# Optimization experiments

Hardware: AMD Instinct MI355X
Metric: run time of the kernel (lower is better)

## Reference

```python
import jax, jax.numpy as jnp
import numpy as np

K = 3
STRIDE = 1
PAD = 1

def conv2d(x, w, b, stride, padding):
    out = jax.lax.conv_general_dilated(x, w, (stride, stride), [(padding, padding), (padding, padding)],
                                       dimension_numbers=('NCHW', 'OIHW', 'NCHW'))
    if b is not None:
        out = out + b[None, :, None, None]
    return out

def deform_conv2d(x, offset, mask, weight, stride, padding):
    # torchvision-style modulated deformable conv (offset_groups=1, groups=1)
    B, C, H, W = x.shape
    C2 = weight.shape[0]
    KK = K * K
    Hout, Wout = offset.shape[2], offset.shape[3]
    off = offset.reshape(B, KK, 2, Hout, Wout)  # (dy, dx) pairs per kernel tap
    ky = jnp.repeat(jnp.arange(K), K)  # kernel row per tap [KK]
    kx = jnp.tile(jnp.arange(K), K)    # kernel col per tap [KK]
    base_y = (jnp.arange(Hout) * stride - padding).astype(jnp.float32)
    base_x = (jnp.arange(Wout) * stride - padding).astype(jnp.float32)
    py = off[:, :, 0] + ky[None, :, None, None] + base_y[None, None, :, None]  # [B,KK,Hout,Wout]
    px = off[:, :, 1] + kx[None, :, None, None] + base_x[None, None, None, :]
    y0f = jnp.floor(py); x0f = jnp.floor(px)
    ly = py - y0f; lx = px - x0f
    y0 = y0f.astype(jnp.int32); x0 = x0f.astype(jnp.int32)
    xf = x.reshape(B, C, H * W)

    def corner(yi, xi, wgt):
        valid = (yi >= 0) & (yi < H) & (xi >= 0) & (xi < W)
        idx = (jnp.clip(yi, 0, H - 1) * W + jnp.clip(xi, 0, W - 1)).reshape(B, -1)  # [B, KK*Hout*Wout]
        v = jax.vmap(lambda xb, ib: xb[:, ib])(xf, idx)  # [B, C, KK*Hout*Wout]
        return v * (wgt * valid).reshape(B, 1, -1)

    val = (corner(y0, x0, (1.0 - ly) * (1.0 - lx))
           + corner(y0, x0 + 1, (1.0 - ly) * lx)
           + corner(y0 + 1, x0, ly * (1.0 - lx))
           + corner(y0 + 1, x0 + 1, ly * lx))
    val = val * mask.reshape(B, 1, -1)  # modulation per (tap, spatial)
    val = val.reshape(B, C, KK, Hout, Wout)
    out = jnp.einsum('bckhw,ock->bohw', val, weight.reshape(C2, C, KK))
    return out

def setup_inputs() -> dict:
    key = jax.random.key(0)
    ks = jax.random.split(key, 6)
    B, C1, C2, H, W = 8, 256, 256, 64, 64
    x = jax.random.normal(ks[0], (B, C1, H, W), jnp.float32)
    offset_w = jax.random.normal(ks[1], (2 * K * K, C1, K, K), jnp.float32) * 0.01
    offset_b = jax.random.normal(ks[2], (2 * K * K,), jnp.float32) * 0.5
    mod_w = jax.random.normal(ks[3], (K * K, C1, K, K), jnp.float32) * 0.01
    mod_b = jnp.zeros((K * K,), jnp.float32)
    reg_w = jax.random.normal(ks[4], (C2, C1, K, K), jnp.float32) * np.float32(1.0 / np.sqrt(C1 * K * K))
    return {"x": x, "offset_w": offset_w, "offset_b": offset_b, "mod_w": mod_w, "mod_b": mod_b, "reg_w": reg_w}

def reference(x, offset_w, offset_b, mod_w, mod_b, reg_w):
    h, w = x.shape[2], x.shape[3]
    max_offset = max(h, w) / 4.0
    offset = jnp.clip(conv2d(x, offset_w, offset_b, STRIDE, PAD), -max_offset, max_offset)
    modulator = jax.nn.sigmoid(conv2d(x, mod_w, mod_b, STRIDE, PAD))
    return deform_conv2d(x, offset, modulator, reg_w, STRIDE, PAD)
```

## Files before the change

kernel.cpp:

```cpp
#include <hip/hip_runtime.h>
#include <math.h>

#define BB 8
#define CIN 256
#define COUT 256
#define HH 64
#define WW 64
#define OCM 27
#define KTOT 2304
#define NKT 72

typedef unsigned int u32;
typedef unsigned short u16;
typedef _Float16 f16;

#define WS_XBF 0
#define WS_W2 16777216
#define WS_W2OM 17956864
#define WS_OFFMOD 18104320

__device__ __forceinline__ u16 f2h(float f) {
    f16 h = (f16)f;
    return __builtin_bit_cast(u16, h);
}

typedef __attribute__((address_space(1))) const unsigned int* gptr_t;
typedef __attribute__((address_space(3))) unsigned int* lptr_t;
__device__ __forceinline__ void gl2lds16(const void* g, void* l) {
    __builtin_amdgcn_global_load_lds((gptr_t)g, (lptr_t)l, 16, 0, 0);
}

typedef __attribute__((ext_vector_type(8))) f16 frag;
typedef __attribute__((ext_vector_type(2))) f16 h2;
typedef __attribute__((ext_vector_type(4))) float f4;

__device__ __forceinline__ int sw_off(int row, int oct) {
    return (row << 5) + ((oct ^ ((row >> 1) & 3)) << 3);
}

#define BARRIER_RAW() do { asm volatile("" ::: "memory"); \
    __builtin_amdgcn_s_barrier(); asm volatile("" ::: "memory"); } while (0)

__global__ __launch_bounds__(256) void k_nhwc3(const float* __restrict__ x,
                                               u16* __restrict__ xbf) {
    const int y = blockIdx.x, b = blockIdx.y;
    __shared__ float T[64][65];
    const int t = threadIdx.x;
    const int wl = t & 63, g = t >> 6;
    const int pr = wl & 31, wsub = wl >> 5;
    u32* xo = (u32*)xbf;
    for (int c0 = 0; c0 < 256; c0 += 64) {
#pragma unroll
        for (int i = 0; i < 16; ++i) {
            int c = g + i * 4;
            T[c][wl] = x[(((size_t)(b * 256 + c0 + c)) << 12) + (y << 6) + wl];
        }
        __syncthreads();
#pragma unroll
        for (int j = 0; j < 8; ++j) {
            int w = j * 8 + g * 2 + wsub;
            u32 v = (u32)f2h(T[2 * pr][w]) | ((u32)f2h(T[2 * pr + 1][w]) << 16);
            xo[((((size_t)b << 12) + (y << 6) + w) << 7) + (c0 >> 1) + pr] = v;
        }
        __syncthreads();
    }
}

__global__ void k_pack_w2(const float* __restrict__ rw, u16* __restrict__ w2) {
    int o = blockIdx.x * blockDim.x + threadIdx.x;
    if (o >= NKT * COUT * 32) return;
    int kk = o & 31;
    int n = (o >> 5) & 255;
    int kt = o >> 13;
    int k = kt * 32 + kk;
    int tap = k >> 8;
    int c = k & 255;
    w2[o] = f2h(rw[n * KTOT + c * 9 + tap]);
}

__global__ void k_pack_w2om(const float* __restrict__ ow, const float* __restrict__ mw,
                            u16* __restrict__ w2om) {
    int o = blockIdx.x * blockDim.x + threadIdx.x;
    if (o >= NKT * 32 * 32) return;
    int kk = o & 31;
    int oc = (o >> 5) & 31;
    int kt = o >> 10;
    int k = kt * 32 + kk;
    int tap = k >> 8;
    int c = k & 255;
    float v = 0.f;
    if (oc < 18) v = ow[oc * KTOT + c * 9 + tap];
    else if (oc < 27) v = mw[(oc - 18) * KTOT + c * 9 + tap];
    w2om[o] = f2h(v);
}

__global__ __launch_bounds__(512, 4) void k_offmod6(
    const u16* __restrict__ xbf, const u16* __restrict__ w2om,
    const float* __restrict__ ob, const float* __restrict__ mb,
    float* __restrict__ offmod)
{
    const int b = blockIdx.x & 7, h = blockIdx.x >> 3;
    const int t = threadIdx.x;
    const int lane = t & 63, wv = t >> 6;
    const int hf = wv >> 2;
    const int wl4 = wv & 3;
    const int th = t & 255;
    const int fr = lane & 15, q = lane >> 4;
    const int wm = wl4 << 4;
    const int mg = th >> 2, oct = th & 3;

    __shared__ u16 AsB[2][2][64 * 32];
    __shared__ u16 BsB[2][2][32 * 32];
    __shared__ float red[64][33];

    const u16* xb = xbf + ((size_t)b << 20);
    const int kbase = hf * 36;

    auto loadA = [&](int kt, uint4* r) {
        int tap = kt >> 3;
        int yy = h + tap / 3 - 1, xx = mg + tap % 3 - 1;
        int c0 = ((kt & 7) << 5) + (oct << 3);
        uint4 v = make_uint4(0, 0, 0, 0);
        if ((unsigned)yy < HH && (unsigned)xx < WW)
            v = *(const uint4*)(xb + (((size_t)yy << 6) + xx) * 256 + c0);
        *r = v;
    };
    auto loadB = [&](int kt, uint4* r) {
        if (th < 128) *r = *(const uint4*)(w2om + (size_t)kt * 1024 + (th >> 2) * 32 + (th & 3) * 8);
    };
    auto storeAB = [&](int buf, uint4* rA, uint4* rB) {
        *(uint4*)&AsB[hf][buf][sw_off(mg, oct)] = *rA;
        if (th < 128) *(uint4*)&BsB[hf][buf][sw_off(th >> 2, th & 3)] = *rB;
    };

    f4 acc[2];
    acc[0] = (f4){0.f, 0.f, 0.f, 0.f};
    acc[1] = (f4){0.f, 0.f, 0.f, 0.f};

    uint4 rA0, rB0, rA1, rB1;
    loadA(kbase, &rA0); loadB(kbase, &rB0);
    storeAB(0, &rA0, &rB0);
    loadA(kbase + 1, &rA1); loadB(kbase + 1, &rB1);
    asm volatile("s_waitcnt lgkmcnt(0)" ::: "memory");

    auto body = [&](int i, int p, uint4* cA, uint4* cB, uint4* nA, uint4* nB) {
        BARRIER_RAW();
        frag a  = *(const frag*)&AsB[hf][p][sw_off(wm + fr, q)];
        frag b0 = *(const frag*)&BsB[hf][p][sw_off(fr, q)];
        frag b1 = *(const frag*)&BsB[hf][p][sw_off(16 + fr, q)];
        if (i + 2 < 36) { loadA(kbase + i + 2, nA); loadB(kbase + i + 2, nB); }
        if (i + 1 < 36) storeAB(1 - p, cA, cB);
        acc[0] = __builtin_amdgcn_mfma_f32_16x16x32_f16(a, b0, acc[0], 0, 0, 0);
        acc[1] = __builtin_amdgcn_mfma_f32_16x16x32_f16(a, b1, acc[1], 0, 0, 0);
        asm volatile("s_waitcnt lgkmcnt(0)" ::: "memory");
    };
    for (int i = 0; i < 36; i += 2) {
        body(i, 0, &rA1, &rB1, &rA0, &rB0);
        body(i + 1, 1, &rA0, &rB0, &rA1, &rB1);
    }

    if (hf == 1) {
#pragma unroll
        for (int ni = 0; ni < 2; ++ni)
#pragma unroll
            for (int r = 0; r < 4; ++r)
                red[wm + q * 4 + r][ni * 16 + fr] = acc[ni][r];
    }
    __syncthreads();
    if (hf == 0) {
#pragma unroll
        for (int ni = 0; ni < 2; ++ni) {
            int oc = ni * 16 + fr;
            if (oc >= OCM) continue;
            bool is_off = oc < 18;
            float bias = is_off ? ob[oc] : mb[oc - 18];
            float4 v;
            float* vp = (float*)&v;
#pragma unroll
            for (int r = 0; r < 4; ++r) {
                float s = acc[ni][r] + red[wm + q * 4 + r][oc] + bias;
                vp[r] = is_off ? fminf(fmaxf(s, -16.f), 16.f)
                               : 1.f / (1.f + __expf(-s));
            }
            *(float4*)&offmod[(((size_t)b * OCM + oc) << 12) + (h << 6) + wm + q * 4] = v;
        }
    }
}

__global__ __launch_bounds__(1024, 4) void k_deform8(
    const u16* __restrict__ xbf, const float* __restrict__ offmod,
    const u16* __restrict__ w2, float* __restrict__ out)
{
    const int t = threadIdx.x;
    const int b = blockIdx.x & 7, hp = blockIdx.x >> 3;
    const int h0 = hp << 1;
    const int lane = t & 63, wv = t >> 6;

    __shared__ uint4 STAB[9][128];
    __shared__ u16 AsB[2][128 * 32];
    __shared__ u16 BsB[2][256 * 32];

    const float* om = offmod + (size_t)b * OCM * 4096;
    for (int e = t; e < 9 * 128; e += 1024) {
        int m = e & 127, tap = e >> 7;
        int hh = h0 + (m >> 6), ww = m & 63;
        float dy = om[(tap * 2) * 4096 + hh * 64 + ww];
        float dx = om[(tap * 2 + 1) * 4096 + hh * 64 + ww];
        float mv = om[(18 + tap) * 4096 + hh * 64 + ww];
        float py = dy + (float)(tap / 3) + (float)(hh - 1);
        float px = dx + (float)(tap % 3) + (float)(ww - 1);
        float y0f = floorf(py), x0f = floorf(px);
        float ly = py - y0f, lx = px - x0f;
        int y0 = (int)y0f, x0 = (int)x0f;
        int   ysr[2] = {y0, y0 + 1};
        int   xsr[2] = {x0, x0 + 1};
        float wy[2] = {1.f - ly, ly};
        float wx[2] = {1.f - lx, lx};
        u16 idx[4]; f16 wgt[4];
#pragma unroll
        for (int r = 0; r < 4; ++r) {
            int yy = ysr[r >> 1], xx = xsr[r & 1];
            bool ok = ((unsigned)yy < HH) && ((unsigned)xx < WW);
            int yc = min(max(yy, 0), HH - 1);
            int xc = min(max(xx, 0), WW - 1);
            idx[r] = (u16)(yc * WW + xc);
            wgt[r] = (f16)(ok ? (wy[r >> 1] * wx[r & 1] * mv) : 0.f);
        }
        uint4 tv;
        tv.x = (u32)idx[0] | ((u32)idx[1] << 16);
        tv.y = (u32)idx[2] | ((u32)idx[3] << 16);
        h2 w01 = {wgt[0], wgt[1]};
        h2 w23 = {wgt[2], wgt[3]};
        tv.z = __builtin_bit_cast(u32, w01);
        tv.w = __builtin_bit_cast(u32, w23);
        STAB[tap][m] = tv;
    }
    __syncthreads();

    if (wv < 8) {
        const int fr = lane & 15, q = lane >> 4;
        const int wn = wv << 5;

        f4 acc[8][2];
#pragma unroll
        for (int mi = 0; mi < 8; ++mi) {
            acc[mi][0] = (f4){0.f, 0.f, 0.f, 0.f};
            acc[mi][1] = (f4){0.f, 0.f, 0.f, 0.f};
        }

        for (int kt = 0; kt < NKT; ++kt) {
            const int p = kt & 1;
            BARRIER_RAW();
            frag b0 = *(const frag*)&BsB[p][sw_off(wn + fr, q)];
            frag b1 = *(const frag*)&BsB[p][sw_off(wn + 16 + fr, q)];
#pragma unroll
            for (int mi = 0; mi < 8; ++mi) {
                frag a = *(const frag*)&AsB[p][sw_off(mi * 16 + fr, q)];
                acc[mi][0] = __builtin_amdgcn_mfma_f32_16x16x32_f16(a, b0, acc[mi][0], 0, 0, 0);
                acc[mi][1] = __builtin_amdgcn_mfma_f32_16x16x32_f16(a, b1, acc[mi][1], 0, 0, 0);
            }
        }

#pragma unroll
        for (int ni = 0; ni < 2; ++ni) {
            int n_g = wn + ni * 16 + fr;
            float* outn = out + (((size_t)b * COUT + n_g) << 12) + (h0 << 6);
#pragma unroll
            for (int mi = 0; mi < 8; ++mi) {
                int off = ((mi >> 2) << 6) + ((mi & 3) << 4) + (q << 2);
                *(float4*)&outn[off] = make_float4(acc[mi][ni][0], acc[mi][ni][1],
                                                   acc[mi][ni][2], acc[mi][ni][3]);
            }
        }
    } else {
        const int pt = t - 512;
        const int mg = pt >> 2, oct = pt & 3;
        const int pwv = wv - 8;
        const int ko_sw = (lane & 3) ^ ((lane >> 3) & 3);
        const u16* xpl = xbf + ((size_t)b << 20);

        auto stageB = [&](int kt, int buf) {
            const u16* src = w2 + ((size_t)kt << 13);
#pragma unroll
            for (int j = 0; j < 2; ++j) {
                int base = (pwv << 5) + (j << 4);
                int n = base + (lane >> 2);
                u16* dst = &BsB[buf][base << 5];
                gl2lds16(src + n * 32 + ko_sw * 8, dst);
            }
        };
        auto loadCorners = [&](int kt, uint4 (&cr)[4]) {
            int tap = kt >> 3;
            int c0 = ((kt & 7) << 5) + (oct << 3);
            uint2 iv = *(const uint2*)&STAB[tap][mg];
            const u16* base = xpl + c0;
            cr[0] = *(const uint4*)(base + ((size_t)(iv.x & 0xFFFFu) << 8));
            cr[1] = *(const uint4*)(base + ((size_t)(iv.x >> 16) << 8));
            cr[2] = *(const uint4*)(base + ((size_t)(iv.y & 0xFFFFu) << 8));
            cr[3] = *(const uint4*)(base + ((size_t)(iv.y >> 16) << 8));
        };
        auto interpStore = [&](int kt, int buf, uint4 (&cr)[4]) {
            int tap = kt >> 3;
            uint2 wvp = *(const uint2*)(((const u32*)&STAB[tap][mg]) + 2);
            h2 w01 = __builtin_bit_cast(h2, wvp.x);
            h2 w23 = __builtin_bit_cast(h2, wvp.y);
            h2 s0 = {w01[0], w01[0]};
            h2 s1 = {w01[1], w01[1]};
            h2 s2 = {w23[0], w23[0]};
            h2 s3 = {w23[1], w23[1]};
            const u32* c0p = (const u32*)&cr[0];
            const u32* c1p = (const u32*)&cr[1];
            const u32* c2p = (const u32*)&cr[2];
            const u32* c3p = (const u32*)&cr[3];
            u32 o[4];
#pragma unroll
            for (int jj = 0; jj < 4; ++jj) {
                h2 v = s0 * __builtin_bit_cast(h2, c0p[jj]);
                v += s1 * __builtin_bit_cast(h2, c1p[jj]);
                v += s2 * __builtin_bit_cast(h2, c2p[jj]);
                v += s3 * __builtin_bit_cast(h2, c3p[jj]);
                o[jj] = __builtin_bit_cast(u32, v);
            }
            *(uint4*)&AsB[buf][sw_off(mg, oct)] = make_uint4(o[0], o[1], o[2], o[3]);
        };

        uint4 cr0[4], cr1[4], cr2[4];
        stageB(0, 0);
        loadCorners(0, cr0);
        loadCorners(1, cr1);
        loadCorners(2, cr2);
        interpStore(0, 0, cr0);
        asm volatile("s_waitcnt lgkmcnt(0)" ::: "memory");

        auto pstep = [&](int kt, int p, uint4 (&cur)[4], uint4 (&nxt)[4]) {
            if (kt + 2 < NKT) asm volatile("s_waitcnt vmcnt(4)" ::: "memory");
            else              asm volatile("s_waitcnt vmcnt(0)" ::: "memory");
            BARRIER_RAW();
            if (kt + 1 < NKT) stageB(kt + 1, 1 - p);
            if (kt + 3 < NKT) loadCorners(kt + 3, nxt);
            if (kt + 1 < NKT) interpStore(kt + 1, 1 - p, cur);
            asm volatile("s_waitcnt lgkmcnt(0)" ::: "memory");
        };
        for (int kt = 0; kt < NKT; kt += 6) {
            pstep(kt,     0, cr1, cr0);
            pstep(kt + 1, 1, cr2, cr1);
            pstep(kt + 2, 0, cr0, cr2);
            pstep(kt + 3, 1, cr1, cr0);
            pstep(kt + 4, 0, cr2, cr1);
            pstep(kt + 5, 1, cr0, cr2);
        }
    }
}

extern "C" void kernel_launch(void* const* d_in, const int* in_sizes, int n_in,
                              void* d_out, int out_size, void* d_ws, size_t ws_size,
                              hipStream_t stream) {
    const float* x  = (const float*)d_in[0];
    const float* ow = (const float*)d_in[1];
    const float* ob = (const float*)d_in[2];
    const float* mw = (const float*)d_in[3];
    const float* mb = (const float*)d_in[4];
    const float* rw = (const float*)d_in[5];
    float* out = (float*)d_out;
    char* ws = (char*)d_ws;

    u16*   xbf    = (u16*)(ws + WS_XBF);
    u16*   w2     = (u16*)(ws + WS_W2);
    u16*   w2om   = (u16*)(ws + WS_W2OM);
    float* offmod = (float*)(ws + WS_OFFMOD);

    k_nhwc3<<<dim3(HH, BB), 256, 0, stream>>>(x, xbf);
    k_pack_w2<<<(NKT * COUT * 32 + 255) / 256, 256, 0, stream>>>(rw, w2);
    k_pack_w2om<<<(NKT * 32 * 32 + 255) / 256, 256, 0, stream>>>(ow, mw, w2om);
    k_offmod6<<<dim3(512), 512, 0, stream>>>(xbf, w2om, ob, mb, offmod);
    k_deform8<<<dim3(256), 1024, 0, stream>>>(xbf, offmod, w2, out);
}
```

Baseline: 169.8 us.

## Fuse prep kernels into one launch and retile deform MFMA warps 4x4

```diff
diff --git a/kernel.cpp b/kernel.cpp
--- a/kernel.cpp
+++ b/kernel.cpp
@@ -41,57 +41,56 @@
 #define BARRIER_RAW() do { asm volatile("" ::: "memory"); \
     __builtin_amdgcn_s_barrier(); asm volatile("" ::: "memory"); } while (0)
 
-__global__ __launch_bounds__(256) void k_nhwc3(const float* __restrict__ x,
-                                               u16* __restrict__ xbf) {
-    const int y = blockIdx.x, b = blockIdx.y;
-    __shared__ float T[64][65];
+__global__ __launch_bounds__(256) void k_prep(
+    const float* __restrict__ x, const float* __restrict__ rw,
+    const float* __restrict__ ow, const float* __restrict__ mw,
+    u16* __restrict__ xbf, u16* __restrict__ w2, u16* __restrict__ w2om)
+{
+    const int bid = blockIdx.x;
     const int t = threadIdx.x;
-    const int wl = t & 63, g = t >> 6;
-    const int pr = wl & 31, wsub = wl >> 5;
-    u32* xo = (u32*)xbf;
-    for (int c0 = 0; c0 < 256; c0 += 64) {
-#pragma unroll
-        for (int i = 0; i < 16; ++i) {
-            int c = g + i * 4;
-            T[c][wl] = x[(((size_t)(b * 256 + c0 + c)) << 12) + (y << 6) + wl];
-        }
-        __syncthreads();
-#pragma unroll
-        for (int j = 0; j < 8; ++j) {
-            int w = j * 8 + g * 2 + wsub;
-            u32 v = (u32)f2h(T[2 * pr][w]) | ((u32)f2h(T[2 * pr + 1][w]) << 16);
-            xo[((((size_t)b << 12) + (y << 6) + w) << 7) + (c0 >> 1) + pr] = v;
-        }
-        __syncthreads();
-    }
-}
-
-__global__ void k_pack_w2(const float* __restrict__ rw, u16* __restrict__ w2) {
-    int o = blockIdx.x * blockDim.x + threadIdx.x;
-    if (o >= NKT * COUT * 32) return;
-    int kk = o & 31;
-    int n = (o >> 5) & 255;
-    int kt = o >> 13;
-    int k = kt * 32 + kk;
-    int tap = k >> 8;
-    int c = k & 255;
-    w2[o] = f2h(rw[n * KTOT + c * 9 + tap]);
-}
-
-__global__ void k_pack_w2om(const float* __restrict__ ow, const float* __restrict__ mw,
-                            u16* __restrict__ w2om) {
-    int o = blockIdx.x * blockDim.x + threadIdx.x;
-    if (o >= NKT * 32 * 32) return;
-    int kk = o & 31;
-    int oc = (o >> 5) & 31;
-    int kt = o >> 10;
-    int k = kt * 32 + kk;
-    int tap = k >> 8;
-    int c = k & 255;
-    float v = 0.f;
-    if (oc < 18) v = ow[oc * KTOT + c * 9 + tap];
-    else if (oc < 27) v = mw[(oc - 18) * KTOT + c * 9 + tap];
-    w2om[o] = f2h(v);
+    if (bid < 512) {
+        const int y = bid & 63, b = bid >> 6;
+        __shared__ float T[64][65];
+        const int wl = t & 63, g = t >> 6;
+        const int pr = wl & 31, wsub = wl >> 5;
+        u32* xo = (u32*)xbf;
+        for (int c0 = 0; c0 < 256; c0 += 64) {
+#pragma unroll
+            for (int i = 0; i < 16; ++i) {
+                int c = g + i * 4;
+                T[c][wl] = x[(((size_t)(b * 256 + c0 + c)) << 12) + (y << 6) + wl];
+            }
+            __syncthreads();
+#pragma unroll
+            for (int j = 0; j < 8; ++j) {
+                int w = j * 8 + g * 2 + wsub;
+                u32 v = (u32)f2h(T[2 * pr][w]) | ((u32)f2h(T[2 * pr + 1][w]) << 16);
+                xo[((((size_t)b << 12) + (y << 6) + w) << 7) + (c0 >> 1) + pr] = v;
+            }
+            __syncthreads();
+        }
+    } else if (bid < 2816) {
+        int o = ((bid - 512) << 8) + t;
+        int kk = o & 31;
+        int n = (o >> 5) & 255;
+        int kt = o >> 13;
+        int k = kt * 32 + kk;
+        int tap = k >> 8;
+        int c = k & 255;
+        w2[o] = f2h(rw[n * KTOT + c * 9 + tap]);
+    } else {
+        int o = ((bid - 2816) << 8) + t;
+        int kk = o & 31;
+        int oc = (o >> 5) & 31;
+        int kt = o >> 10;
+        int k = kt * 32 + kk;
+        int tap = k >> 8;
+        int c = k & 255;
+        float v = 0.f;
+        if (oc < 18) v = ow[oc * KTOT + c * 9 + tap];
+        else if (oc < 27) v = mw[(oc - 18) * KTOT + c * 9 + tap];
+        w2om[o] = f2h(v);
+    }
 }
 
 __global__ __launch_bounds__(512, 4) void k_offmod6(
@@ -187,7 +186,7 @@
     }
 }
 
-__global__ __launch_bounds__(1024, 4) void k_deform8(
+__global__ __launch_bounds__(1024, 4) void k_deform9(
     const u16* __restrict__ xbf, const float* __restrict__ offmod,
     const u16* __restrict__ w2, float* __restrict__ out)
 {
@@ -239,37 +238,44 @@
 
     if (wv < 8) {
         const int fr = lane & 15, q = lane >> 4;
-        const int wn = wv << 5;
-
-        f4 acc[8][2];
-#pragma unroll
-        for (int mi = 0; mi < 8; ++mi) {
-            acc[mi][0] = (f4){0.f, 0.f, 0.f, 0.f};
-            acc[mi][1] = (f4){0.f, 0.f, 0.f, 0.f};
-        }
+        const int wn4 = wv & 3;
+        const int wm2 = wv >> 2;
+
+        f4 acc[4][4];
+#pragma unroll
+        for (int mi = 0; mi < 4; ++mi)
+#pragma unroll
+            for (int ni = 0; ni < 4; ++ni) acc[mi][ni] = (f4){0.f, 0.f, 0.f, 0.f};
 
         for (int kt = 0; kt < NKT; ++kt) {
             const int p = kt & 1;
             BARRIER_RAW();
-            frag b0 = *(const frag*)&BsB[p][sw_off(wn + fr, q)];
-            frag b1 = *(const frag*)&BsB[p][sw_off(wn + 16 + fr, q)];
-#pragma unroll
-            for (int mi = 0; mi < 8; ++mi) {
-                frag a = *(const frag*)&AsB[p][sw_off(mi * 16 + fr, q)];
-                acc[mi][0] = __builtin_amdgcn_mfma_f32_16x16x32_f16(a, b0, acc[mi][0], 0, 0, 0);
-                acc[mi][1] = __builtin_amdgcn_mfma_f32_16x16x32_f16(a, b1, acc[mi][1], 0, 0, 0);
-            }
-        }
-
-#pragma unroll
-        for (int ni = 0; ni < 2; ++ni) {
-            int n_g = wn + ni * 16 + fr;
-            float* outn = out + (((size_t)b * COUT + n_g) << 12) + (h0 << 6);
-#pragma unroll
-            for (int mi = 0; mi < 8; ++mi) {
-                int off = ((mi >> 2) << 6) + ((mi & 3) << 4) + (q << 2);
-                *(float4*)&outn[off] = make_float4(acc[mi][ni][0], acc[mi][ni][1],
-                                                   acc[mi][ni][2], acc[mi][ni][3]);
+            frag av[4], bv[4];
+#pragma unroll
+            for (int mi = 0; mi < 4; ++mi)
+                av[mi] = *(const frag*)&AsB[p][sw_off((wm2 << 6) + mi * 16 + fr, q)];
+#pragma unroll
+            for (int ni = 0; ni < 4; ++ni)
+                bv[ni] = *(const frag*)&BsB[p][sw_off((wn4 << 6) + ni * 16 + fr, q)];
+            __builtin_amdgcn_s_setprio(1);
+#pragma unroll
+            for (int mi = 0; mi < 4; ++mi)
+#pragma unroll
+                for (int ni = 0; ni < 4; ++ni)
+                    acc[mi][ni] = __builtin_amdgcn_mfma_f32_16x16x32_f16(
+                        av[mi], bv[ni], acc[mi][ni], 0, 0, 0);
+            __builtin_amdgcn_s_setprio(0);
+        }
+
+#pragma unroll
+        for (int ni = 0; ni < 4; ++ni) {
+            int n_g = (wn4 << 6) + ni * 16 + fr;
+            float* outn = out + (((size_t)b * COUT + n_g) << 12) + ((h0 + wm2) << 6);
+#pragma unroll
+            for (int mi = 0; mi < 4; ++mi) {
+                *(float4*)&outn[mi * 16 + (q << 2)] =
+                    make_float4(acc[mi][ni][0], acc[mi][ni][1],
+                                acc[mi][ni][2], acc[mi][ni][3]);
             }
         }
     } else {
@@ -369,9 +375,7 @@
     u16*   w2om   = (u16*)(ws + WS_W2OM);
     float* offmod = (float*)(ws + WS_OFFMOD);
 
-    k_nhwc3<<<dim3(HH, BB), 256, 0, stream>>>(x, xbf);
-    k_pack_w2<<<(NKT * COUT * 32 + 255) / 256, 256, 0, stream>>>(rw, w2);
-    k_pack_w2om<<<(NKT * 32 * 32 + 255) / 256, 256, 0, stream>>>(ow, mw, w2om);
+    k_prep<<<dim3(3104), 256, 0, stream>>>(x, rw, ow, mw, xbf, w2, w2om);
     k_offmod6<<<dim3(512), 512, 0, stream>>>(xbf, w2om, ob, mb, offmod);
-    k_deform8<<<dim3(256), 1024, 0, stream>>>(xbf, offmod, w2, out);
-}
+    k_deform9<<<dim3(256), 1024, 0, stream>>>(xbf, offmod, w2, out);
+}
```

Result: faster. 165.0 us (-2.8%).

## Fuse offset/mask conv into deform kernel and merge prep kernels

Applied to the files above, without the earlier changes.

```diff
diff --git a/kernel.cpp b/kernel.cpp
--- a/kernel.cpp
+++ b/kernel.cpp
@@ -17,7 +17,6 @@
 #define WS_XBF 0
 #define WS_W2 16777216
 #define WS_W2OM 17956864
-#define WS_OFFMOD 18104320
 
 __device__ __forceinline__ u16 f2h(float f) {
     f16 h = (f16)f;
@@ -41,15 +40,21 @@
 #define BARRIER_RAW() do { asm volatile("" ::: "memory"); \
     __builtin_amdgcn_s_barrier(); asm volatile("" ::: "memory"); } while (0)
 
-__global__ __launch_bounds__(256) void k_nhwc3(const float* __restrict__ x,
-                                               u16* __restrict__ xbf) {
-    const int y = blockIdx.x, b = blockIdx.y;
-    __shared__ float T[64][65];
+__global__ __launch_bounds__(256) void k_prep(
+    const float* __restrict__ x, const float* __restrict__ rw,
+    const float* __restrict__ ow, const float* __restrict__ mw,
+    u16* __restrict__ xbf, u16* __restrict__ w2, u16* __restrict__ w2om)
+{
+    const int bid = blockIdx.x;
     const int t = threadIdx.x;
-    const int wl = t & 63, g = t >> 6;
-    const int pr = wl & 31, wsub = wl >> 5;
-    u32* xo = (u32*)xbf;
-    for (int c0 = 0; c0 < 256; c0 += 64) {
+    if (bid < 2048) {
+        const int c0 = (bid & 3) << 6;
+        const int y = (bid >> 2) & 63;
+        const int b = bid >> 8;
+        __shared__ float T[64][65];
+        const int wl = t & 63, g = t >> 6;
+        const int pr = wl & 31, wsub = wl >> 5;
+        u32* xo = (u32*)xbf;
 #pragma unroll
         for (int i = 0; i < 16; ++i) {
             int c = g + i * 4;
@@ -62,151 +67,138 @@
             u32 v = (u32)f2h(T[2 * pr][w]) | ((u32)f2h(T[2 * pr + 1][w]) << 16);
             xo[((((size_t)b << 12) + (y << 6) + w) << 7) + (c0 >> 1) + pr] = v;
         }
-        __syncthreads();
+    } else if (bid < 4352) {
+        int o = ((bid - 2048) << 8) + t;
+        int kk = o & 31;
+        int n = (o >> 5) & 255;
+        int kt = o >> 13;
+        int k = kt * 32 + kk;
+        int tap = k >> 8;
+        int c = k & 255;
+        w2[o] = f2h(rw[n * KTOT + c * 9 + tap]);
+    } else {
+        int o = ((bid - 4352) << 8) + t;
+        int kk = o & 31;
+        int oc = (o >> 5) & 31;
+        int kt = o >> 10;
+        int k = kt * 32 + kk;
+        int tap = k >> 8;
+        int c = k & 255;
+        float v = 0.f;
+        if (oc < 18) v = ow[oc * KTOT + c * 9 + tap];
+        else if (oc < 27) v = mw[(oc - 18) * KTOT + c * 9 + tap];
+        w2om[o] = f2h(v);
     }
 }
 
-__global__ void k_pack_w2(const float* __restrict__ rw, u16* __restrict__ w2) {
-    int o = blockIdx.x * blockDim.x + threadIdx.x;
-    if (o >= NKT * COUT * 32) return;
-    int kk = o & 31;
-    int n = (o >> 5) & 255;
-    int kt = o >> 13;
-    int k = kt * 32 + kk;
-    int tap = k >> 8;
-    int c = k & 255;
-    w2[o] = f2h(rw[n * KTOT + c * 9 + tap]);
-}
-
-__global__ void k_pack_w2om(const float* __restrict__ ow, const float* __restrict__ mw,
-                            u16* __restrict__ w2om) {
-    int o = blockIdx.x * blockDim.x + threadIdx.x;
-    if (o >= NKT * 32 * 32) return;
-    int kk = o & 31;
-    int oc = (o >> 5) & 31;
-    int kt = o >> 10;
-    int k = kt * 32 + kk;
-    int tap = k >> 8;
-    int c = k & 255;
-    float v = 0.f;
-    if (oc < 18) v = ow[oc * KTOT + c * 9 + tap];
-    else if (oc < 27) v = mw[(oc - 18) * KTOT + c * 9 + tap];
-    w2om[o] = f2h(v);
-}
-
-__global__ __launch_bounds__(512, 4) void k_offmod6(
+__global__ __launch_bounds__(1024, 4) void k_fused(
     const u16* __restrict__ xbf, const u16* __restrict__ w2om,
     const float* __restrict__ ob, const float* __restrict__ mb,
-    float* __restrict__ offmod)
-{
-    const int b = blockIdx.x & 7, h = blockIdx.x >> 3;
-    const int t = threadIdx.x;
-    const int lane = t & 63, wv = t >> 6;
-    const int hf = wv >> 2;
-    const int wl4 = wv & 3;
-    const int th = t & 255;
-    const int fr = lane & 15, q = lane >> 4;
-    const int wm = wl4 << 4;
-    const int mg = th >> 2, oct = th & 3;
-
-    __shared__ u16 AsB[2][2][64 * 32];
-    __shared__ u16 BsB[2][2][32 * 32];
-    __shared__ float red[64][33];
-
-    const u16* xb = xbf + ((size_t)b << 20);
-    const int kbase = hf * 36;
-
-    auto loadA = [&](int kt, uint4* r) {
-        int tap = kt >> 3;
-        int yy = h + tap / 3 - 1, xx = mg + tap % 3 - 1;
-        int c0 = ((kt & 7) << 5) + (oct << 3);
-        uint4 v = make_uint4(0, 0, 0, 0);
-        if ((unsigned)yy < HH && (unsigned)xx < WW)
-            v = *(const uint4*)(xb + (((size_t)yy << 6) + xx) * 256 + c0);
-        *r = v;
-    };
-    auto loadB = [&](int kt, uint4* r) {
-        if (th < 128) *r = *(const uint4*)(w2om + (size_t)kt * 1024 + (th >> 2) * 32 + (th & 3) * 8);
-    };
-    auto storeAB = [&](int buf, uint4* rA, uint4* rB) {
-        *(uint4*)&AsB[hf][buf][sw_off(mg, oct)] = *rA;
-        if (th < 128) *(uint4*)&BsB[hf][buf][sw_off(th >> 2, th & 3)] = *rB;
-    };
-
-    f4 acc[2];
-    acc[0] = (f4){0.f, 0.f, 0.f, 0.f};
-    acc[1] = (f4){0.f, 0.f, 0.f, 0.f};
-
-    uint4 rA0, rB0, rA1, rB1;
-    loadA(kbase, &rA0); loadB(kbase, &rB0);
-    storeAB(0, &rA0, &rB0);
-    loadA(kbase + 1, &rA1); loadB(kbase + 1, &rB1);
-    asm volatile("s_waitcnt lgkmcnt(0)" ::: "memory");
-
-    auto body = [&](int i, int p, uint4* cA, uint4* cB, uint4* nA, uint4* nB) {
-        BARRIER_RAW();
-        frag a  = *(const frag*)&AsB[hf][p][sw_off(wm + fr, q)];
-        frag b0 = *(const frag*)&BsB[hf][p][sw_off(fr, q)];
-        frag b1 = *(const frag*)&BsB[hf][p][sw_off(16 + fr, q)];
-        if (i + 2 < 36) { loadA(kbase + i + 2, nA); loadB(kbase + i + 2, nB); }
-        if (i + 1 < 36) storeAB(1 - p, cA, cB);
-        acc[0] = __builtin_amdgcn_mfma_f32_16x16x32_f16(a, b0, acc[0], 0, 0, 0);
-        acc[1] = __builtin_amdgcn_mfma_f32_16x16x32_f16(a, b1, acc[1], 0, 0, 0);
-        asm volatile("s_waitcnt lgkmcnt(0)" ::: "memory");
-    };
-    for (int i = 0; i < 36; i += 2) {
-        body(i, 0, &rA1, &rB1, &rA0, &rB0);
-        body(i + 1, 1, &rA0, &rB0, &rA1, &rB1);
-    }
-
-    if (hf == 1) {
-#pragma unroll
-        for (int ni = 0; ni < 2; ++ni)
-#pragma unroll
-            for (int r = 0; r < 4; ++r)
-                red[wm + q * 4 + r][ni * 16 + fr] = acc[ni][r];
-    }
-    __syncthreads();
-    if (hf == 0) {
-#pragma unroll
-        for (int ni = 0; ni < 2; ++ni) {
-            int oc = ni * 16 + fr;
-            if (oc >= OCM) continue;
-            bool is_off = oc < 18;
-            float bias = is_off ? ob[oc] : mb[oc - 18];
-            float4 v;
-            float* vp = (float*)&v;
-#pragma unroll
-            for (int r = 0; r < 4; ++r) {
-                float s = acc[ni][r] + red[wm + q * 4 + r][oc] + bias;
-                vp[r] = is_off ? fminf(fmaxf(s, -16.f), 16.f)
-                               : 1.f / (1.f + __expf(-s));
-            }
-            *(float4*)&offmod[(((size_t)b * OCM + oc) << 12) + (h << 6) + wm + q * 4] = v;
-        }
-    }
-}
-
-__global__ __launch_bounds__(1024, 4) void k_deform8(
-    const u16* __restrict__ xbf, const float* __restrict__ offmod,
     const u16* __restrict__ w2, float* __restrict__ out)
 {
     const int t = threadIdx.x;
     const int b = blockIdx.x & 7, hp = blockIdx.x >> 3;
     const int h0 = hp << 1;
     const int lane = t & 63, wv = t >> 6;
-
-    __shared__ uint4 STAB[9][128];
-    __shared__ u16 AsB[2][128 * 32];
-    __shared__ u16 BsB[2][256 * 32];
-
-    const float* om = offmod + (size_t)b * OCM * 4096;
+    const int fr = lane & 15, q = lane >> 4;
+
+    __shared__ __align__(16) char SMEM[81520];
+    uint4* STAB = (uint4*)SMEM;
+    float* RED  = (float*)SMEM;
+    u16* As  = (u16*)(SMEM + 18432);
+    u16* Bs  = (u16*)(SMEM + 18432 + 16384);
+    u16* Aom = (u16*)(SMEM + 18432);
+    u16* Bom = (u16*)(SMEM + 18432 + 32768);
+    float* OM = (float*)(SMEM + 67584);
+
+    const u16* xb = xbf + ((size_t)b << 20);
+
+    {
+        const int half = t >> 9;
+        const int tl = t & 511;
+        const int mg1 = tl >> 2, oct1 = tl & 3;
+        const int wm1 = ((t >> 6) & 7) << 4;
+        const int kb1 = half * 36;
+
+        auto loadA1 = [&](int kt, uint4* r) {
+            int tap = kt >> 3;
+            int yy = h0 + (mg1 >> 6) + tap / 3 - 1;
+            int xx = (mg1 & 63) + tap % 3 - 1;
+            int c0 = ((kt & 7) << 5) + (oct1 << 3);
+            uint4 v = make_uint4(0, 0, 0, 0);
+            if ((unsigned)yy < HH && (unsigned)xx < WW)
+                v = *(const uint4*)(xb + (((size_t)yy << 6) + xx) * 256 + c0);
+            *r = v;
+        };
+        auto loadB1 = [&](int kt, uint4* r) {
+            if (tl < 128) *r = *(const uint4*)(w2om + (size_t)kt * 1024 + (tl >> 2) * 32 + (tl & 3) * 8);
+        };
+        auto storeAB1 = [&](int buf, uint4* rA, uint4* rB) {
+            *(uint4*)&Aom[(((half << 1) | buf) << 12) + sw_off(mg1, oct1)] = *rA;
+            if (tl < 128)
+                *(uint4*)&Bom[(((half << 1) | buf) << 10) + sw_off(tl >> 2, tl & 3)] = *rB;
+        };
+
+        f4 acc1[2];
+        acc1[0] = (f4){0.f, 0.f, 0.f, 0.f};
+        acc1[1] = (f4){0.f, 0.f, 0.f, 0.f};
+
+        uint4 rA0, rB0, rA1, rB1;
+        loadA1(kb1, &rA0); loadB1(kb1, &rB0);
+        storeAB1(0, &rA0, &rB0);
+        loadA1(kb1 + 1, &rA1); loadB1(kb1 + 1, &rB1);
+        asm volatile("s_waitcnt lgkmcnt(0)" ::: "memory");
+
+        auto body1 = [&](int i, int p, uint4* cA, uint4* cB, uint4* nA, uint4* nB) {
+            BARRIER_RAW();
+            frag a  = *(const frag*)&Aom[(((half << 1) | p) << 12) + sw_off(wm1 + fr, q)];
+            frag b0 = *(const frag*)&Bom[(((half << 1) | p) << 10) + sw_off(fr, q)];
+            frag b1 = *(const frag*)&Bom[(((half << 1) | p) << 10) + sw_off(16 + fr, q)];
+            if (i + 2 < 36) { loadA1(kb1 + i + 2, nA); loadB1(kb1 + i + 2, nB); }
+            if (i + 1 < 36) storeAB1(1 - p, cA, cB);
+            acc1[0] = __builtin_amdgcn_mfma_f32_16x16x32_f16(a, b0, acc1[0], 0, 0, 0);
+            acc1[1] = __builtin_amdgcn_mfma_f32_16x16x32_f16(a, b1, acc1[1], 0, 0, 0);
+            asm volatile("s_waitcnt lgkmcnt(0)" ::: "memory");
+        };
+        for (int i = 0; i < 36; i += 2) {
+            body1(i, 0, &rA1, &rB1, &rA0, &rB0);
+            body1(i + 1, 1, &rA0, &rB0, &rA1, &rB1);
+        }
+
+        if (half == 1) {
+#pragma unroll
+            for (int ni = 0; ni < 2; ++ni)
+#pragma unroll
+                for (int r = 0; r < 4; ++r)
+                    RED[(wm1 + q * 4 + r) * 33 + ni * 16 + fr] = acc1[ni][r];
+        }
+        __syncthreads();
+        if (half == 0) {
+#pragma unroll
+            for (int ni = 0; ni < 2; ++ni) {
+                int oc = ni * 16 + fr;
+                if (oc < OCM) {
+                    bool is_off = oc < 18;
+                    float bias = is_off ? ob[oc] : mb[oc - 18];
+#pragma unroll
+                    for (int r = 0; r < 4; ++r) {
+                        float s = acc1[ni][r] + RED[(wm1 + q * 4 + r) * 33 + oc] + bias;
+                        OM[oc * 129 + wm1 + q * 4 + r] =
+                            is_off ? fminf(fmaxf(s, -16.f), 16.f)
+                                   : 1.f / (1.f + __expf(-s));
+                    }
+                }
+            }
+        }
+        __syncthreads();
+    }
+
     for (int e = t; e < 9 * 128; e += 1024) {
         int m = e & 127, tap = e >> 7;
         int hh = h0 + (m >> 6), ww = m & 63;
-        float dy = om[(tap * 2) * 4096 + hh * 64 + ww];
-        float dx = om[(tap * 2 + 1) * 4096 + hh * 64 + ww];
-        float mv = om[(18 + tap) * 4096 + hh * 64 + ww];
+        float dy = OM[(tap * 2) * 129 + m];
+        float dx = OM[(tap * 2 + 1) * 129 + m];
+        float mv = OM[(18 + tap) * 129 + m];
         float py = dy + (float)(tap / 3) + (float)(hh - 1);
         float px = dx + (float)(tap % 3) + (float)(ww - 1);
         float y0f = floorf(py), x0f = floorf(px);
@@ -233,12 +225,11 @@
         h2 w23 = {wgt[2], wgt[3]};
         tv.z = __builtin_bit_cast(u32, w01);
         tv.w = __builtin_bit_cast(u32, w23);
-        STAB[tap][m] = tv;
+        STAB[tap * 128 + m] = tv;
     }
     __syncthreads();
 
     if (wv < 8) {
-        const int fr = lane & 15, q = lane >> 4;
         const int wn = wv << 5;
 
         f4 acc[8][2];
@@ -251,11 +242,11 @@
         for (int kt = 0; kt < NKT; ++kt) {
             const int p = kt & 1;
             BARRIER_RAW();
-            frag b0 = *(const frag*)&BsB[p][sw_off(wn + fr, q)];
-            frag b1 = *(const frag*)&BsB[p][sw_off(wn + 16 + fr, q)];
+            frag b0 = *(const frag*)&Bs[(p << 13) + sw_off(wn + fr, q)];
+            frag b1 = *(const frag*)&Bs[(p << 13) + sw_off(wn + 16 + fr, q)];
 #pragma unroll
             for (int mi = 0; mi < 8; ++mi) {
-                frag a = *(const frag*)&AsB[p][sw_off(mi * 16 + fr, q)];
+                frag a = *(const frag*)&As[(p << 12) + sw_off(mi * 16 + fr, q)];
                 acc[mi][0] = __builtin_amdgcn_mfma_f32_16x16x32_f16(a, b0, acc[mi][0], 0, 0, 0);
                 acc[mi][1] = __builtin_amdgcn_mfma_f32_16x16x32_f16(a, b1, acc[mi][1], 0, 0, 0);
             }
@@ -267,9 +258,9 @@
             float* outn = out + (((size_t)b * COUT + n_g) << 12) + (h0 << 6);
 #pragma unroll
             for (int mi = 0; mi < 8; ++mi) {
-                int off = ((mi >> 2) << 6) + ((mi & 3) << 4) + (q << 2);
-                *(float4*)&outn[off] = make_float4(acc[mi][ni][0], acc[mi][ni][1],
-                                                   acc[mi][ni][2], acc[mi][ni][3]);
+                *(float4*)&outn[mi * 16 + (q << 2)] =
+                    make_float4(acc[mi][ni][0], acc[mi][ni][1],
+                                acc[mi][ni][2], acc[mi][ni][3]);
             }
         }
     } else {
@@ -277,7 +268,6 @@
         const int mg = pt >> 2, oct = pt & 3;
         const int pwv = wv - 8;
         const int ko_sw = (lane & 3) ^ ((lane >> 3) & 3);
-        const u16* xpl = xbf + ((size_t)b << 20);
 
         auto stageB = [&](int kt, int buf) {
             const u16* src = w2 + ((size_t)kt << 13);
@@ -285,15 +275,15 @@
             for (int j = 0; j < 2; ++j) {
                 int base = (pwv << 5) + (j << 4);
                 int n = base + (lane >> 2);
-                u16* dst = &BsB[buf][base << 5];
+                u16* dst = &Bs[(buf << 13) + (base << 5)];
                 gl2lds16(src + n * 32 + ko_sw * 8, dst);
             }
         };
         auto loadCorners = [&](int kt, uint4 (&cr)[4]) {
             int tap = kt >> 3;
             int c0 = ((kt & 7) << 5) + (oct << 3);
-            uint2 iv = *(const uint2*)&STAB[tap][mg];
-            const u16* base = xpl + c0;
+            uint2 iv = *(const uint2*)&STAB[tap * 128 + mg];
+            const u16* base = xb + c0;
             cr[0] = *(const uint4*)(base + ((size_t)(iv.x & 0xFFFFu) << 8));
             cr[1] = *(const uint4*)(base + ((size_t)(iv.x >> 16) << 8));
             cr[2] = *(const uint4*)(base + ((size_t)(iv.y & 0xFFFFu) << 8));
@@ -301,7 +291,7 @@
         };
         auto interpStore = [&](int kt, int buf, uint4 (&cr)[4]) {
             int tap = kt >> 3;
-            uint2 wvp = *(const uint2*)(((const u32*)&STAB[tap][mg]) + 2);
+            uint2 wvp = *(const uint2*)(((const u32*)&STAB[tap * 128 + mg]) + 2);
             h2 w01 = __builtin_bit_cast(h2, wvp.x);
             h2 w23 = __builtin_bit_cast(h2, wvp.y);
             h2 s0 = {w01[0], w01[0]};
@@ -321,7 +311,7 @@
                 v += s3 * __builtin_bit_cast(h2, c3p[jj]);
                 o[jj] = __builtin_bit_cast(u32, v);
             }
-            *(uint4*)&AsB[buf][sw_off(mg, oct)] = make_uint4(o[0], o[1], o[2], o[3]);
+            *(uint4*)&As[(buf << 12) + sw_off(mg, oct)] = make_uint4(o[0], o[1], o[2], o[3]);
         };
 
         uint4 cr0[4], cr1[4], cr2[4];
@@ -364,14 +354,10 @@
     float* out = (float*)d_out;
     char* ws = (char*)d_ws;
 
-    u16*   xbf    = (u16*)(ws + WS_XBF);
-    u16*   w2     = (u16*)(ws + WS_W2);
-    u16*   w2om   = (u16*)(ws + WS_W2OM);
-    float* offmod = (float*)(ws + WS_OFFMOD);
-
-    k_nhwc3<<<dim3(HH, BB), 256, 0, stream>>>(x, xbf);
-    k_pack_w2<<<(NKT * COUT * 32 + 255) / 256, 256, 0, stream>>>(rw, w2);
-    k_pack_w2om<<<(NKT * 32 * 32 + 255) / 256, 256, 0, stream>>>(ow, mw, w2om);
-    k_offmod6<<<dim3(512), 512, 0, stream>>>(xbf, w2om, ob, mb, offmod);
-    k_deform8<<<dim3(256), 1024, 0, stream>>>(xbf, offmod, w2, out);
-}
+    u16* xbf  = (u16*)(ws + WS_XBF);
+    u16* w2   = (u16*)(ws + WS_W2);
+    u16* w2om = (u16*)(ws + WS_W2OM);
+
+    k_prep<<<dim3(4640), 256, 0, stream>>>(x, rw, ow, mw, xbf, w2, w2om);
+    k_fused<<<dim3(256), 1024, 0, stream>>>(xbf, w2om, ob, mb, w2, out);
+}
```

Measured after the change: 171.5 us. No clear change (+1.0%).
